# Kernel optimization log

Measured on AMD Instinct MI355X. Metric: run time of the kernel, lower is better.

Reference implementation:

```python
import jax, jax.numpy as jnp
import numpy as np
import math

B, T, C, H = 2, 2048, 1024, 16

def setup_inputs() -> dict:
    key = jax.random.key(0)
    ks = jax.random.split(key, 5)
    s = 0.02
    return {
        "x": jax.random.normal(ks[0], (B, T, C), dtype=jnp.float32),
        "W_attn": jax.random.normal(ks[1], (C, 3 * C), dtype=jnp.float32) * s,
        "b_attn": jnp.zeros((3 * C,), dtype=jnp.float32),
        "W_proj": jax.random.normal(ks[2], (C, C), dtype=jnp.float32) * s,
        "b_proj": jnp.zeros((C,), dtype=jnp.float32),
    }

def reference(x, W_attn, b_attn, W_proj, b_proj):
    Bx, Tx, Cx = x.shape
    hd = Cx // H  # head dim = 64
    qkv = x @ W_attn + b_attn                      # [B,T,3C]
    q, k, v = jnp.split(qkv, 3, axis=-1)
    # [B,H,T,hd]
    q = q.reshape(Bx, Tx, H, hd).transpose(0, 2, 1, 3)
    k = k.reshape(Bx, Tx, H, hd).transpose(0, 2, 1, 3)
    v = v.reshape(Bx, Tx, H, hd).transpose(0, 2, 1, 3)
    scale = 1.0 / math.sqrt(hd)
    att = jnp.einsum('bhqd,bhkd->bhqk', q, k) * scale   # [B,H,T,T]
    causal = jnp.tril(jnp.ones((Tx, Tx), dtype=bool))
    att = jnp.where(causal[None, None, :, :], att, -jnp.inf)
    att = jax.nn.softmax(att, axis=-1)
    y = jnp.einsum('bhqk,bhkd->bhqd', att, v)           # [B,H,T,hd]
    y = y.transpose(0, 2, 1, 3).reshape(Bx, Tx, Cx)
    return y @ W_proj + b_proj
```

## Files before the change

### kernel.cpp

```cpp
#include <hip/hip_runtime.h>

typedef __attribute__((ext_vector_type(8))) __bf16 bf16x8;
typedef __attribute__((ext_vector_type(4))) float f32x4;

#define T_SEQ 2048
#define NH 16
#define HD 64
#define CDIM 1024
#define NQK 2048
#define NQKV 3072
#define MTOT 4096

#define SWZ(r, c) ((((r) * 8) + ((c) ^ ((r) & 7))) * 8)

__device__ __forceinline__ void async_load16(const void* g, void* l) {
    __builtin_amdgcn_global_load_lds(
        (const __attribute__((address_space(1))) void*)g,
        (__attribute__((address_space(3))) void*)l, 16, 0, 0);
}

__global__ __launch_bounds__(256) void cvt_bf16_kernel(const float* __restrict__ in,
                                                       __bf16* __restrict__ out, int n) {
    int i = (blockIdx.x * 256 + threadIdx.x) * 8;
    if (i + 8 <= n) {
        float4 f0 = *(const float4*)(in + i);
        float4 f1 = *(const float4*)(in + i + 4);
        bf16x8 o;
        o[0] = (__bf16)f0.x; o[1] = (__bf16)f0.y; o[2] = (__bf16)f0.z; o[3] = (__bf16)f0.w;
        o[4] = (__bf16)f1.x; o[5] = (__bf16)f1.y; o[6] = (__bf16)f1.z; o[7] = (__bf16)f1.w;
        *(bf16x8*)(out + i) = o;
    }
}

__global__ __launch_bounds__(256) void transpose2_kernel(
    const float* __restrict__ Wa, const float* __restrict__ Wp,
    __bf16* __restrict__ WaT, __bf16* __restrict__ WpT) {
    __shared__ float tile[32][33];
    const float* in; __bf16* out; int C, bx = blockIdx.x;
    if (bx < 96) { in = Wa; out = WaT; C = 3072; }
    else         { in = Wp; out = WpT; C = 1024; bx -= 96; }
    int c0 = bx * 32, r0 = blockIdx.y * 32;
    int tx = threadIdx.x, ty = threadIdx.y;
#pragma unroll
    for (int i = 0; i < 4; i++)
        tile[ty + i * 8][tx] = in[(size_t)(r0 + ty + i * 8) * C + c0 + tx];
    __syncthreads();
#pragma unroll
    for (int i = 0; i < 4; i++)
        out[(size_t)(c0 + ty + i * 8) * 1024 + r0 + tx] = (__bf16)tile[tx][ty + i * 8];
}

template <int WNW>
__global__ __launch_bounds__(256) void gemm_bt_kernel(
    const __bf16* __restrict__ A, const __bf16* __restrict__ Bt,
    const float* __restrict__ bias, int M, int N, int K, int mode,
    __bf16* __restrict__ qkb, __bf16* __restrict__ vtb, float* __restrict__ outf)
{
    constexpr int MI = (WNW == 2) ? 4 : 2;
    constexpr int BROWS = WNW * 64;
    __shared__ __bf16 As[128 * 64];
    __shared__ __bf16 Bs[BROWS * 64];

    int tid = threadIdx.x;
    int lane = tid & 63, wid = tid >> 6;
    int quad = lane >> 4, r16 = lane & 15;
    int wm = (WNW == 2) ? (wid >> 1) * 64 : wid * 32;
    int wn = (WNW == 2) ? (wid & 1) * 64 : 0;
    int bm = blockIdx.y * 128, bn = blockIdx.x * (WNW * 64);

    f32x4 acc[MI][4] = {};

    int lrow = lane >> 3;
    int lcolsw = (((lane & 7) ^ (lrow & 7)) * 8);
    const __bf16* Ag = A + (size_t)(bm + wid * 32 + lrow) * K + lcolsw;
    const __bf16* Bg = Bt + (size_t)(bn + wid * (BROWS / 4) + lrow) * K + lcolsw;
    char* lA = (char*)As + wid * 4096;
    char* lB = (char*)Bs + wid * (BROWS / 4) * 128;

    for (int kt = 0; kt < K; kt += 64) {
        __syncthreads();
#pragma unroll
        for (int i = 0; i < 4; i++)
            async_load16(Ag + kt + (size_t)i * 8 * K, lA + i * 1024);
#pragma unroll
        for (int i = 0; i < BROWS / 32; i++)
            async_load16(Bg + kt + (size_t)i * 8 * K, lB + i * 1024);
        __syncthreads();
#pragma unroll
        for (int ks = 0; ks < 2; ks++) {
            bf16x8 af[MI], bfr[4];
#pragma unroll
            for (int i = 0; i < MI; i++)
                af[i] = *(const bf16x8*)&As[SWZ(wm + i * 16 + r16, ks * 4 + quad)];
#pragma unroll
            for (int i = 0; i < 4; i++)
                bfr[i] = *(const bf16x8*)&Bs[SWZ(wn + i * 16 + r16, ks * 4 + quad)];
#pragma unroll
            for (int mi = 0; mi < MI; mi++)
#pragma unroll
                for (int ni = 0; ni < 4; ni++)
                    acc[mi][ni] = __builtin_amdgcn_mfma_f32_16x16x32_bf16(
                        af[mi], bfr[ni], acc[mi][ni], 0, 0, 0);
        }
    }

    const float SC2 = 0.125f * 1.44269504088896f;
#pragma unroll
    for (int mi = 0; mi < MI; mi++) {
#pragma unroll
        for (int ni = 0; ni < 4; ni++) {
            int col = bn + wn + ni * 16 + r16;
            float bv = bias[col];
            int row0 = bm + wm + mi * 16 + quad * 4;
            if (mode == 1) {
#pragma unroll
                for (int rg = 0; rg < 4; rg++)
                    outf[(size_t)(row0 + rg) * N + col] = acc[mi][ni][rg] + bv;
            } else if (col < 1024) {
#pragma unroll
                for (int rg = 0; rg < 4; rg++)
                    qkb[(size_t)(row0 + rg) * NQK + col] = (__bf16)((acc[mi][ni][rg] + bv) * SC2);
            } else if (col < 2048) {
#pragma unroll
                for (int rg = 0; rg < 4; rg++)
                    qkb[(size_t)(row0 + rg) * NQK + col] = (__bf16)(acc[mi][ni][rg] + bv);
            } else {
                int dcol = col - 2048;
                int b = row0 >> 11, t0 = row0 & 2047;
                union { __bf16 h[4]; uint2 u; } pk;
#pragma unroll
                for (int rg = 0; rg < 4; rg++) pk.h[rg] = (__bf16)(acc[mi][ni][rg] + bv);
                *(uint2*)&vtb[((size_t)b * 1024 + dcol) * T_SEQ + t0] = pk.u;
            }
        }
    }
}

__global__ __launch_bounds__(256) void attn_kernel(
    const __bf16* __restrict__ qkb, const __bf16* __restrict__ vtb,
    __bf16* __restrict__ y1)
{
    __shared__ __bf16 Ks[2][64 * 64];
    __shared__ __bf16 Vs[2][64 * 64];
    __shared__ __bf16 Ps[4][16][72];

    int tid = threadIdx.x;
    int lane = tid & 63, w = tid >> 6;
    int quad = lane >> 4, r16 = lane & 15;
    int bh = blockIdx.y;
    int b = bh >> 4, h = bh & 15;
    int qtA = blockIdx.x, qtB = 31 - qtA;
    int qbA = qtA * 64, qbB = qtB * 64;

    const __bf16* Qh = qkb + (size_t)b * T_SEQ * NQK + h * HD;
    const __bf16* Kh = Qh + CDIM;
    const __bf16* Vh = vtb + ((size_t)b * 1024 + h * HD) * T_SEQ;

    const float NEG_INF = -__builtin_inff();
    int lrow = lane >> 3;
    int lcolsw = (((lane & 7) ^ (lrow & 7)) * 8);

    bf16x8 qfA[2], qfB[2];
#pragma unroll
    for (int ks = 0; ks < 2; ks++) {
        qfA[ks] = *(const bf16x8*)(Qh + (size_t)(qbA + w * 16 + r16) * NQK + ks * 32 + quad * 8);
        qfB[ks] = *(const bf16x8*)(Qh + (size_t)(qbB + w * 16 + r16) * NQK + ks * 32 + quad * 8);
    }
    f32x4 oA[4] = {}, oB[4] = {};
    float lA_ = 0.f, lB_ = 0.f;
    int g0A = qbA + w * 16, g0B = qbB + w * 16;
    int qrowA = g0A + r16, qrowB = g0B + r16;

    auto stage = [&](int kt, int buf) {
        int kb = kt * 64;
        char* lK = (char*)Ks[buf] + w * 2048;
        char* lV = (char*)Vs[buf] + w * 2048;
        const __bf16* kg = Kh + (size_t)(kb + w * 16 + lrow) * NQK + lcolsw;
        const __bf16* vg = Vh + (size_t)(w * 16 + lrow) * T_SEQ + kb + lcolsw;
        async_load16(kg, lK);
        async_load16(kg + (size_t)8 * NQK, lK + 1024);
        async_load16(vg, lV);
        async_load16(vg + (size_t)8 * T_SEQ, lV + 1024);
    };

    auto tile_compute = [&](int kb, int buf, const bf16x8 (&qf)[2], f32x4 (&o)[4],
                            float& l_i, int g0, int qrow) {
        f32x4 s[4] = {};
#pragma unroll
        for (int ks = 0; ks < 2; ks++) {
            bf16x8 kf[4];
#pragma unroll
            for (int ni = 0; ni < 4; ni++)
                kf[ni] = *(const bf16x8*)&Ks[buf][SWZ(ni * 16 + r16, ks * 4 + quad)];
#pragma unroll
            for (int ni = 0; ni < 4; ni++)
                s[ni] = __builtin_amdgcn_mfma_f32_16x16x32_bf16(kf[ni], qf[ks], s[ni], 0, 0, 0);
        }
        if (kb + 63 > g0) {
#pragma unroll
            for (int ni = 0; ni < 4; ni++)
#pragma unroll
                for (int rg = 0; rg < 4; rg++)
                    if (kb + ni * 16 + quad * 4 + rg > qrow) s[ni][rg] = NEG_INF;
        }
#pragma unroll
        for (int ni = 0; ni < 4; ni++)
#pragma unroll
            for (int rg = 0; rg < 4; rg++) {
                float p = exp2f(s[ni][rg]);
                s[ni][rg] = p;
                l_i += p;
            }
#pragma unroll
        for (int ni = 0; ni < 4; ni++) {
            union { __bf16 h[4]; uint2 u; } pk;
#pragma unroll
            for (int rg = 0; rg < 4; rg++) pk.h[rg] = (__bf16)s[ni][rg];
            *(uint2*)&Ps[w][r16][ni * 16 + quad * 4] = pk.u;
        }
#pragma unroll
        for (int ks = 0; ks < 2; ks++) {
            bf16x8 vf[4];
#pragma unroll
            for (int nd = 0; nd < 4; nd++)
                vf[nd] = *(const bf16x8*)&Vs[buf][SWZ(nd * 16 + r16, ks * 4 + quad)];
            bf16x8 pb = *(const bf16x8*)&Ps[w][r16][ks * 32 + quad * 8];
#pragma unroll
            for (int nd = 0; nd < 4; nd++)
                o[nd] = __builtin_amdgcn_mfma_f32_16x16x32_bf16(vf[nd], pb, o[nd], 0, 0, 0);
        }
    };

    int nktA = qtA + 1, nktB = qtB + 1;
    stage(0, 0);
    int cur = 0;
    for (int kt = 0; kt < nktB; kt++) {
        __syncthreads();
        if (kt + 1 < nktB) stage(kt + 1, cur ^ 1);
        int kb = kt * 64;
        tile_compute(kb, cur, qfB, oB, lB_, g0B, qrowB);
        if (kt < nktA)
            tile_compute(kb, cur, qfA, oA, lA_, g0A, qrowA);
        cur ^= 1;
    }

#pragma unroll
    for (int which = 0; which < 2; which++) {
        f32x4* o = which ? oB : oA;
        float rs = which ? lB_ : lA_;
        rs += __shfl_xor(rs, 16, 64);
        rs += __shfl_xor(rs, 32, 64);
        float inv = 1.f / rs;
        int t = (which ? qbB : qbA) + w * 16 + r16;
#pragma unroll
        for (int nd = 0; nd < 4; nd++) {
            union { __bf16 h[4]; uint2 u; } pk;
#pragma unroll
            for (int rg = 0; rg < 4; rg++) pk.h[rg] = (__bf16)(o[nd][rg] * inv);
            *(uint2*)&y1[(size_t)(b * T_SEQ + t) * CDIM + h * HD + nd * 16 + quad * 4] = pk.u;
        }
    }
}

extern "C" void kernel_launch(void* const* d_in, const int* in_sizes, int n_in,
                              void* d_out, int out_size, void* d_ws, size_t ws_size,
                              hipStream_t stream) {
    const float* x = (const float*)d_in[0];
    const float* W_attn = (const float*)d_in[1];
    const float* b_attn = (const float*)d_in[2];
    const float* W_proj = (const float*)d_in[3];
    const float* b_proj = (const float*)d_in[4];
    float* out = (float*)d_out;

    char* p = (char*)d_ws;
    __bf16* xb = (__bf16*)p;   p += (size_t)MTOT * CDIM * 2;
    __bf16* WaT = (__bf16*)p;  p += (size_t)3 * CDIM * CDIM * 2;
    __bf16* WpT = (__bf16*)p;  p += (size_t)CDIM * CDIM * 2;
    __bf16* qkb = (__bf16*)p;  p += (size_t)MTOT * NQK * 2;
    __bf16* vtb = (__bf16*)p;  p += (size_t)2 * 1024 * T_SEQ * 2;
    __bf16* y1 = xb;

    cvt_bf16_kernel<<<2048, 256, 0, stream>>>(x, xb, MTOT * CDIM);
    transpose2_kernel<<<dim3(128, 32), dim3(32, 8), 0, stream>>>(W_attn, W_proj, WaT, WpT);
    gemm_bt_kernel<2><<<dim3(24, 32), 256, 0, stream>>>(xb, WaT, b_attn, MTOT, NQKV, CDIM, 0,
                                                        qkb, vtb, nullptr);
    attn_kernel<<<dim3(16, 32), 256, 0, stream>>>(qkb, vtb, y1);
    gemm_bt_kernel<1><<<dim3(16, 32), 256, 0, stream>>>(y1, WpT, b_proj, MTOT, CDIM, CDIM, 1,
                                                        nullptr, nullptr, out);
}
```

Baseline: 185.4 us.

## Split attention KV loop across two blocks and combine partials in separate kernel

The attention kernel gains a grid z-dimension of 2. Each block handles alternating KV tiles and writes unnormalized fp32 partial outputs and row sums, and a new combine kernel adds the partials, normalizes and writes bf16. This doubles block count to improve CU occupancy on the 256-CU part, but it drops the LDS double buffering (now single buffer with a sync after the load) and adds fp32 partial traffic plus an extra launch. It stays correct because the softmax uses no running max, so partials add directly. The d_out buffer serves as scratch for one partial before the final GEMM overwrites it.

```diff
diff --git a/kernel.cpp b/kernel.cpp
--- a/kernel.cpp
+++ b/kernel.cpp
@@ -138,10 +138,10 @@
 
 __global__ __launch_bounds__(256) void attn_kernel(
     const __bf16* __restrict__ qkb, const __bf16* __restrict__ vtb,
-    __bf16* __restrict__ y1)
+    float* __restrict__ oP0, float* __restrict__ oP1, float* __restrict__ lP)
 {
-    __shared__ __bf16 Ks[2][64 * 64];
-    __shared__ __bf16 Vs[2][64 * 64];
+    __shared__ __bf16 Ks[64 * 64];
+    __shared__ __bf16 Vs[64 * 64];
     __shared__ __bf16 Ps[4][16][72];
 
     int tid = threadIdx.x;
@@ -149,6 +149,7 @@
     int quad = lane >> 4, r16 = lane & 15;
     int bh = blockIdx.y;
     int b = bh >> 4, h = bh & 15;
+    int z = blockIdx.z;
     int qtA = blockIdx.x, qtB = 31 - qtA;
     int qbA = qtA * 64, qbB = qtB * 64;
 
@@ -159,6 +160,8 @@
     const float NEG_INF = -__builtin_inff();
     int lrow = lane >> 3;
     int lcolsw = (((lane & 7) ^ (lrow & 7)) * 8);
+    char* lK = (char*)Ks + w * 2048;
+    char* lV = (char*)Vs + w * 2048;
 
     bf16x8 qfA[2], qfB[2];
 #pragma unroll
@@ -171,95 +174,106 @@
     int g0A = qbA + w * 16, g0B = qbB + w * 16;
     int qrowA = g0A + r16, qrowB = g0B + r16;
 
-    auto stage = [&](int kt, int buf) {
+    auto tile_compute = [&](int kb, const bf16x8 (&qf)[2], f32x4 (&o)[4],
+                            float& l_i, int g0, int qrow) {
+        f32x4 s[4] = {};
+#pragma unroll
+        for (int ks = 0; ks < 2; ks++) {
+            bf16x8 kf[4];
+#pragma unroll
+            for (int ni = 0; ni < 4; ni++)
+                kf[ni] = *(const bf16x8*)&Ks[SWZ(ni * 16 + r16, ks * 4 + quad)];
+#pragma unroll
+            for (int ni = 0; ni < 4; ni++)
+                s[ni] = __builtin_amdgcn_mfma_f32_16x16x32_bf16(kf[ni], qf[ks], s[ni], 0, 0, 0);
+        }
+        if (kb + 63 > g0) {
+#pragma unroll
+            for (int ni = 0; ni < 4; ni++)
+#pragma unroll
+                for (int rg = 0; rg < 4; rg++)
+                    if (kb + ni * 16 + quad * 4 + rg > qrow) s[ni][rg] = NEG_INF;
+        }
+#pragma unroll
+        for (int ni = 0; ni < 4; ni++)
+#pragma unroll
+            for (int rg = 0; rg < 4; rg++) {
+                float p = exp2f(s[ni][rg]);
+                s[ni][rg] = p;
+                l_i += p;
+            }
+#pragma unroll
+        for (int ni = 0; ni < 4; ni++) {
+            union { __bf16 h[4]; uint2 u; } pk;
+#pragma unroll
+            for (int rg = 0; rg < 4; rg++) pk.h[rg] = (__bf16)s[ni][rg];
+            *(uint2*)&Ps[w][r16][ni * 16 + quad * 4] = pk.u;
+        }
+#pragma unroll
+        for (int ks = 0; ks < 2; ks++) {
+            bf16x8 vf[4];
+#pragma unroll
+            for (int nd = 0; nd < 4; nd++)
+                vf[nd] = *(const bf16x8*)&Vs[SWZ(nd * 16 + r16, ks * 4 + quad)];
+            bf16x8 pb = *(const bf16x8*)&Ps[w][r16][ks * 32 + quad * 8];
+#pragma unroll
+            for (int nd = 0; nd < 4; nd++)
+                o[nd] = __builtin_amdgcn_mfma_f32_16x16x32_bf16(vf[nd], pb, o[nd], 0, 0, 0);
+        }
+    };
+
+    int nktA = qtA + 1, nktB = qtB + 1;
+    for (int kt = z; kt < nktB; kt += 2) {
         int kb = kt * 64;
-        char* lK = (char*)Ks[buf] + w * 2048;
-        char* lV = (char*)Vs[buf] + w * 2048;
+        __syncthreads();
         const __bf16* kg = Kh + (size_t)(kb + w * 16 + lrow) * NQK + lcolsw;
         const __bf16* vg = Vh + (size_t)(w * 16 + lrow) * T_SEQ + kb + lcolsw;
         async_load16(kg, lK);
         async_load16(kg + (size_t)8 * NQK, lK + 1024);
         async_load16(vg, lV);
         async_load16(vg + (size_t)8 * T_SEQ, lV + 1024);
-    };
-
-    auto tile_compute = [&](int kb, int buf, const bf16x8 (&qf)[2], f32x4 (&o)[4],
-                            float& l_i, int g0, int qrow) {
-        f32x4 s[4] = {};
-#pragma unroll
-        for (int ks = 0; ks < 2; ks++) {
-            bf16x8 kf[4];
-#pragma unroll
-            for (int ni = 0; ni < 4; ni++)
-                kf[ni] = *(const bf16x8*)&Ks[buf][SWZ(ni * 16 + r16, ks * 4 + quad)];
-#pragma unroll
-            for (int ni = 0; ni < 4; ni++)
-                s[ni] = __builtin_amdgcn_mfma_f32_16x16x32_bf16(kf[ni], qf[ks], s[ni], 0, 0, 0);
-        }
-        if (kb + 63 > g0) {
-#pragma unroll
-            for (int ni = 0; ni < 4; ni++)
-#pragma unroll
-                for (int rg = 0; rg < 4; rg++)
-                    if (kb + ni * 16 + quad * 4 + rg > qrow) s[ni][rg] = NEG_INF;
-        }
-#pragma unroll
-        for (int ni = 0; ni < 4; ni++)
-#pragma unroll
-            for (int rg = 0; rg < 4; rg++) {
-                float p = exp2f(s[ni][rg]);
-                s[ni][rg] = p;
-                l_i += p;
-            }
-#pragma unroll
-        for (int ni = 0; ni < 4; ni++) {
-            union { __bf16 h[4]; uint2 u; } pk;
-#pragma unroll
-            for (int rg = 0; rg < 4; rg++) pk.h[rg] = (__bf16)s[ni][rg];
-            *(uint2*)&Ps[w][r16][ni * 16 + quad * 4] = pk.u;
-        }
-#pragma unroll
-        for (int ks = 0; ks < 2; ks++) {
-            bf16x8 vf[4];
-#pragma unroll
-            for (int nd = 0; nd < 4; nd++)
-                vf[nd] = *(const bf16x8*)&Vs[buf][SWZ(nd * 16 + r16, ks * 4 + quad)];
-            bf16x8 pb = *(const bf16x8*)&Ps[w][r16][ks * 32 + quad * 8];
-#pragma unroll
-            for (int nd = 0; nd < 4; nd++)
-                o[nd] = __builtin_amdgcn_mfma_f32_16x16x32_bf16(vf[nd], pb, o[nd], 0, 0, 0);
-        }
-    };
-
-    int nktA = qtA + 1, nktB = qtB + 1;
-    stage(0, 0);
-    int cur = 0;
-    for (int kt = 0; kt < nktB; kt++) {
         __syncthreads();
-        if (kt + 1 < nktB) stage(kt + 1, cur ^ 1);
-        int kb = kt * 64;
-        tile_compute(kb, cur, qfB, oB, lB_, g0B, qrowB);
+
+        tile_compute(kb, qfB, oB, lB_, g0B, qrowB);
         if (kt < nktA)
-            tile_compute(kb, cur, qfA, oA, lA_, g0A, qrowA);
-        cur ^= 1;
-    }
-
+            tile_compute(kb, qfA, oA, lA_, g0A, qrowA);
+    }
+
+    float* oDst = z ? oP1 : oP0;
 #pragma unroll
     for (int which = 0; which < 2; which++) {
         f32x4* o = which ? oB : oA;
         float rs = which ? lB_ : lA_;
         rs += __shfl_xor(rs, 16, 64);
         rs += __shfl_xor(rs, 32, 64);
-        float inv = 1.f / rs;
         int t = (which ? qbB : qbA) + w * 16 + r16;
-#pragma unroll
-        for (int nd = 0; nd < 4; nd++) {
-            union { __bf16 h[4]; uint2 u; } pk;
-#pragma unroll
-            for (int rg = 0; rg < 4; rg++) pk.h[rg] = (__bf16)(o[nd][rg] * inv);
-            *(uint2*)&y1[(size_t)(b * T_SEQ + t) * CDIM + h * HD + nd * 16 + quad * 4] = pk.u;
-        }
-    }
+        int row = b * T_SEQ + t;
+        if (quad == 0) lP[(((size_t)z * 2 + b) * NH + h) * T_SEQ + t] = rs;
+#pragma unroll
+        for (int nd = 0; nd < 4; nd++)
+            *(f32x4*)&oDst[(size_t)row * CDIM + h * HD + nd * 16 + quad * 4] = o[nd];
+    }
+}
+
+__global__ __launch_bounds__(256) void combine_kernel(
+    const float* __restrict__ oP0, const float* __restrict__ oP1,
+    const float* __restrict__ lP, __bf16* __restrict__ y1) {
+    int i = (blockIdx.x * 256 + threadIdx.x) * 8;
+    int row = i >> 10;
+    int col = i & 1023;
+    int h = col >> 6;
+    int b = row >> 11, t = row & 2047;
+    size_t li = ((size_t)(b * NH + h)) * T_SEQ + t;
+    float inv = 1.f / (lP[li] + lP[(size_t)2 * NH * T_SEQ + li]);
+    f32x4 a0 = *(const f32x4*)(oP0 + i), a1 = *(const f32x4*)(oP0 + i + 4);
+    f32x4 b0 = *(const f32x4*)(oP1 + i), b1 = *(const f32x4*)(oP1 + i + 4);
+    bf16x8 y;
+#pragma unroll
+    for (int j = 0; j < 4; j++) {
+        y[j] = (__bf16)((a0[j] + b0[j]) * inv);
+        y[4 + j] = (__bf16)((a1[j] + b1[j]) * inv);
+    }
+    *(bf16x8*)(y1 + i) = y;
 }
 
 extern "C" void kernel_launch(void* const* d_in, const int* in_sizes, int n_in,
@@ -278,13 +292,17 @@
     __bf16* WpT = (__bf16*)p;  p += (size_t)CDIM * CDIM * 2;
     __bf16* qkb = (__bf16*)p;  p += (size_t)MTOT * NQK * 2;
     __bf16* vtb = (__bf16*)p;  p += (size_t)2 * 1024 * T_SEQ * 2;
+    float* oP1 = (float*)p;    p += (size_t)MTOT * CDIM * 4;
+    float* lP = (float*)p;     p += (size_t)2 * 2 * NH * T_SEQ * 4;
+    float* oP0 = out;
     __bf16* y1 = xb;
 
     cvt_bf16_kernel<<<2048, 256, 0, stream>>>(x, xb, MTOT * CDIM);
     transpose2_kernel<<<dim3(128, 32), dim3(32, 8), 0, stream>>>(W_attn, W_proj, WaT, WpT);
     gemm_bt_kernel<2><<<dim3(24, 32), 256, 0, stream>>>(xb, WaT, b_attn, MTOT, NQKV, CDIM, 0,
                                                         qkb, vtb, nullptr);
-    attn_kernel<<<dim3(16, 32), 256, 0, stream>>>(qkb, vtb, y1);
+    attn_kernel<<<dim3(16, 32, 2), 256, 0, stream>>>(qkb, vtb, oP0, oP1, lP);
+    combine_kernel<<<2048, 256, 0, stream>>>(oP0, oP1, lP, y1);
     gemm_bt_kernel<1><<<dim3(16, 32), 256, 0, stream>>>(y1, WpT, b_proj, MTOT, CDIM, CDIM, 1,
                                                         nullptr, nullptr, out);
 }
```

After: 200.1 us. 1.08x slower.
